# Optimization experiments

Hardware: AMD Instinct MI355X
Metric: run time of the kernel (lower is better)

The kernel has to match this reference:

```python
import jax, jax.numpy as jnp
import numpy as np

RESO = 64
VSIZE = 0.3
VOXEL = VSIZE / RESO
HALF = VOXEL / 2.0


def _voxel_xyz():
    line = (np.arange(RESO, dtype=np.float32) * VOXEL + HALF)
    x, y, z = np.meshgrid(line, line, line, indexing='ij')
    return jnp.asarray(np.stack([x, y, z]))  # [3,R,R,R]


def _grid_sample_2d(feats, gx, gy):
    # feats: [NV,C,H,W]; gx,gy: [NV,N] normalized coords (torch align_corners-style)
    NV, C, H, W = feats.shape
    ix = (gx + 1.0) * 0.5 * (W - 1)
    iy = (gy + 1.0) * 0.5 * (H - 1)
    ix0 = jnp.floor(ix); iy0 = jnp.floor(iy)
    ix1 = ix0 + 1.0;     iy1 = iy0 + 1.0
    # bilinear weights from unclamped corners
    w_nw = (ix1 - ix) * (iy1 - iy)
    w_ne = (ix - ix0) * (iy1 - iy)
    w_sw = (ix1 - ix) * (iy - iy0)
    w_se = (ix - ix0) * (iy - iy0)
    mask = ((ix >= 0) & (ix <= W - 1) & (iy >= 0) & (iy <= H - 1)).astype(feats.dtype)
    cx0 = jnp.clip(ix0, 0, W - 1).astype(jnp.int32)
    cx1 = jnp.clip(ix1, 0, W - 1).astype(jnp.int32)
    cy0 = jnp.clip(iy0, 0, H - 1).astype(jnp.int32)
    cy1 = jnp.clip(iy1, 0, H - 1).astype(jnp.int32)
    feats_flat = feats.reshape(NV, C, H * W)  # [NV,C,HW]
    gather = jax.vmap(lambda f, i: f[:, i])   # per-view [C,HW],[N] -> [C,N]
    v_nw = gather(feats_flat, cy0 * W + cx0)
    v_ne = gather(feats_flat, cy0 * W + cx1)
    v_sw = gather(feats_flat, cy1 * W + cx0)
    v_se = gather(feats_flat, cy1 * W + cx1)
    out = (v_nw * w_nw[:, None] + v_ne * w_ne[:, None]
           + v_sw * w_sw[:, None] + v_se * w_se[:, None])  # [NV,C,N]
    return out, mask


def setup_inputs() -> dict:
    key = jax.random.key(0)
    k_feat, k1, k2, k3 = jax.random.split(key, 4)
    NV, C, H, W = 8, 32, 128, 128
    feats = jax.random.normal(k_feat, (NV, C, H, W), dtype=jnp.float32)
    # realistic pinhole intrinsics for a 512x512 image
    K = np.array([[400.0, 0.0, 256.0], [0.0, 400.0, 256.0], [0.0, 0.0, 1.0]], np.float32)
    Ks = jnp.asarray(np.tile(K, (NV, 1, 1)))
    # identity-rotation w2c poses, camera ~0.5m from volume along +z
    poses = []
    for i in range(NV):
        t = np.array([0.02 * (i - 3.5), 0.01 * (i % 2), 0.5 + 0.02 * i], np.float32)
        poses.append(np.concatenate([np.eye(3, dtype=np.float32), t[:, None]], axis=1))
    ref_poses = jnp.asarray(np.stack(poses))
    bbox = jnp.asarray(np.array([[-0.15, -0.15, 0.0], [0.15, 0.15, 0.3]], np.float32))
    W1 = jax.random.normal(k1, (32, 32), dtype=jnp.float32) * 0.1
    W2 = jax.random.normal(k2, (32, 16), dtype=jnp.float32) * 0.1
    W3 = jax.random.normal(k3, (16, 8), dtype=jnp.float32) * 0.1
    return {"feats": feats, "ref_poses": ref_poses, "Ks": Ks, "bbox": bbox,
            "img_h": 512, "img_w": 512,
            "W1": W1, "b1": jnp.zeros((32,), jnp.float32),
            "W2": W2, "b2": jnp.zeros((16,), jnp.float32),
            "W3": W3, "b3": jnp.zeros((8,), jnp.float32)}


def reference(feats, ref_poses, Ks, bbox, img_h, img_w, W1, b1, W2, b2, W3, b3):
    NV, C, H, W = feats.shape
    dt = feats.dtype
    # homogeneous pad of poses and intrinsics
    pose_h = jnp.tile(jnp.eye(4, dtype=dt), (NV, 1, 1)).at[:, :3, :4].set(ref_poses)
    K_pad = jnp.tile(jnp.eye(4, dtype=dt), (NV, 1, 1)).at[:, :3, :3].set(Ks)
    w2pixel = K_pad @ pose_h  # [NV,4,4]
    # voxel centers in world frame
    xyz = _voxel_xyz() + bbox[0][:, None, None, None]  # [3,R,R,R]
    pts = xyz.reshape(3, -1)                            # [3,N], N=R^3
    homo = jnp.concatenate([pts, jnp.ones_like(pts[0:1])], axis=0)  # [4,N]
    pix = jnp.einsum('vij,jn->vin', w2pixel, homo)[:, :3]           # [NV,3,N]
    z = pix[:, 2]                                                    # [NV,N]
    mask_valid_depth = (z > 0).astype(dt)
    uv = pix[:, :2] / z[:, None, :]                                  # [NV,2,N]
    normalizer = jnp.array([img_w, img_h], dtype=dt)
    grid = uv.transpose(0, 2, 1) / normalizer - 1.0                  # [NV,N,2]
    feat, mask = _grid_sample_2d(feats, grid[..., 0], grid[..., 1])  # [NV,C,N],[NV,N]
    mask = mask * mask_valid_depth
    # [NV,C,(X Y Z)] -> [NV,X,Y,Z,C]
    feat = feat.transpose(0, 2, 1).reshape(NV, RESO, RESO, RESO, C)
    mask = mask.reshape(NV, RESO, RESO, RESO)
    # NOTE: original normalizes over dim=1 (NumX), replicated faithfully
    weight = mask / (jnp.sum(mask, axis=1, keepdims=True) + 1e-8)
    weight = weight[..., None]  # [NV,R,R,R,1]
    h1 = jax.nn.relu(feat @ W1 + b1)
    h2 = jax.nn.relu(h1 @ W2 + b2)
    comp = h2 @ W3 + b3  # [NV,R,R,R,8]
    mean = jnp.sum(comp * weight, axis=0, keepdims=True)
    var = jnp.sum(weight * (comp - mean) ** 2, axis=0, keepdims=True)
    mv = jnp.concatenate([mean, var], axis=-1)       # [1,R,R,R,16]
    return jnp.transpose(mv, (0, 4, 3, 2, 1))        # [1,16,Z,Y,X]
```

## Files before the change

### kernel.cpp

```cpp
#include <hip/hip_runtime.h>
#include <math.h>

#define NVIEW 8
#define CIN   32
#define HF    128
#define WF    128
#define C1    32
#define C2    16
#define C3    8
#define RESO  64
#define PLANE (HF*WF)

typedef _Float16 half8_t  __attribute__((ext_vector_type(8)));
typedef _Float16 half2_t  __attribute__((ext_vector_type(2)));
typedef float    floatx4  __attribute__((ext_vector_type(4)));

static __device__ __forceinline__ float vox_coord(int idx, float b) {
    const float VOXEL = (float)(0.3 / 64.0);
    const float HALFV = (float)(0.3 / 128.0);
    return (float)idx * VOXEL + HALFV + b;
}

static __device__ __forceinline__ void proj_ixiy(const float* M, float x, float y, float z,
                                                 float& ix, float& iy, float& zc) {
    float u  = fmaf(M[0], x, fmaf(M[1], y, fmaf(M[2],  z, M[3])));
    float vv = fmaf(M[4], x, fmaf(M[5], y, fmaf(M[6],  z, M[7])));
    zc       = fmaf(M[8], x, fmaf(M[9], y, fmaf(M[10], z, M[11])));
    float invz = __builtin_amdgcn_rcpf(zc);
    ix = u * invz;
    iy = vv * invz;
}

static __device__ __forceinline__ void wave_lds_sync() {
    asm volatile("s_waitcnt lgkmcnt(0)" ::: "memory");
}

__global__ void __launch_bounds__(256) k_g(const float* __restrict__ feats,
                                           const float* __restrict__ W1,
                                           const float* __restrict__ b1,
                                           float4* __restrict__ G4,
                                           const float* __restrict__ Ks,
                                           const float* __restrict__ poses,
                                           const int* __restrict__ ihp,
                                           const int* __restrict__ iwp,
                                           const float* __restrict__ W2,
                                           const float* __restrict__ b2,
                                           const float* __restrict__ W3,
                                           const float* __restrict__ b3,
                                           float* __restrict__ mats,
                                           _Float16* __restrict__ w2f,
                                           _Float16* __restrict__ w3f,
                                           float* __restrict__ b2f,
                                           float* __restrict__ b3f) {
    if (blockIdx.x == 512) {
        int t = threadIdx.x;
        if (t < NVIEW * 12) {
            int v = t / 12, rc = t % 12, r = rc / 4, c = rc % 4;
            const float* K = Ks + v * 9;
            const float* P = poses + v * 12;
            float s = K[r*3+0]*P[0*4+c] + K[r*3+1]*P[1*4+c] + K[r*3+2]*P[2*4+c];
            float sc = (r == 0) ? 63.5f / (float)iwp[0]
                     : (r == 1) ? 63.5f / (float)ihp[0] : 1.0f;
            mats[v*12 + r*4 + c] = s * sc;
        }
        if (t < 64) {
            int n = t & 15, g = t >> 4;
#pragma unroll
            for (int jj = 0; jj < 8; jj++) {
                int kk = 8 * g + jj;
                w2f[t*8 + jj] = (_Float16)W2[kk * C2 + n];
                float w3v = (kk < C2 && n < C3) ? W3[kk * C3 + n] : 0.0f;
                w3f[t*8 + jj] = (_Float16)w3v;
            }
            b2f[t] = b2[n];
            b3f[t] = (n < C3) ? b3[n] : 0.0f;
        }
        return;
    }
    int t = blockIdx.x * 256 + threadIdx.x;
    int pix = t & (PLANE - 1);
    int v = t >> 14;
    const float* fp = feats + ((size_t)v * CIN) * PLANE + pix;
    float f[CIN];
#pragma unroll
    for (int c = 0; c < CIN; c++) f[c] = fp[(size_t)c * PLANE];
    float g[C1];
#pragma unroll
    for (int jj = 0; jj < C1; jj++) g[jj] = b1[jj];
#pragma unroll
    for (int c = 0; c < CIN; c++) {
        float fc = f[c];
#pragma unroll
        for (int jj = 0; jj < C1; jj++) g[jj] = fmaf(fc, W1[c*C1 + jj], g[jj]);
    }
#pragma unroll
    for (int q = 0; q < C1/4; q++)
        G4[((size_t)(v * 8 + q)) * PLANE + pix] =
            make_float4(g[4*q], g[4*q+1], g[4*q+2], g[4*q+3]);
}

__global__ void __launch_bounds__(256) k_main(
    const float4* __restrict__ G4,
    const float* __restrict__ mats, const float* __restrict__ bbox,
    const _Float16* __restrict__ w2f, const _Float16* __restrict__ w3f,
    const float* __restrict__ b2f, const float* __restrict__ b3f,
    float* __restrict__ out) {
    __shared__ __align__(16) _Float16 h2s[4][64 * 24];

    int tid  = threadIdx.x;
    int wv   = tid >> 6;
    int lane = tid & 63;
    int col  = blockIdx.x * 4 + wv;
    int j  = col & 63;
    int kz = col >> 6;
    _Float16* h2b = h2s[wv];

    int m = lane & 15, g = lane >> 4;
    float y = vox_coord(j, bbox[1]);
    float z = vox_coord(kz, bbox[2]);

    half8_t w2frag = *(const half8_t*)(w2f + lane * 8);
    half8_t w3frag = *(const half8_t*)(w3f + lane * 8);
    float b2c = b2f[lane];
    float b3c = b3f[lane];
    floatx4 cb2 = {b2c, b2c, b2c, b2c};
    floatx4 cb3 = {b3c, b3c, b3c, b3c};

    float M1[16], Msq[16], S16[16];
#pragma unroll
    for (int c = 0; c < 16; c++) { M1[c] = 0.0f; Msq[c] = 0.0f; S16[c] = 0.0f; }

#pragma unroll 1
    for (int v = 0; v < NVIEW; v++) {
        const float* M = mats + v * 12;
        const float4* Gv = G4 + (size_t)v * 8 * PLANE;

        floatx4 c2v[4];
        unsigned int ballo[4];
        int popc = 0;

#pragma unroll
        for (int T = 0; T < 4; T++) {
            int ipt = T * 16 + m;
            float x = vox_coord(ipt, bbox[0]);
            float ix, iy, zc;
            proj_ixiy(M, x, y, z, ix, iy, zc);

            float fx0 = floorf(ix), fy0 = floorf(iy);
            float fx1 = fx0 + 1.0f, fy1 = fy0 + 1.0f;
            bool inb = (ix >= 0.0f) && (ix <= (float)(WF-1)) &&
                       (iy >= 0.0f) && (iy <= (float)(HF-1)) && (zc > 0.0f);
            int cx0 = (int)fminf(fmaxf(fx0, 0.0f), (float)(WF-1));
            int cx1 = (int)fminf(fmaxf(fx1, 0.0f), (float)(WF-1));
            int cy0 = (int)fminf(fmaxf(fy0, 0.0f), (float)(HF-1));
            int cy1 = (int)fminf(fmaxf(fy1, 0.0f), (float)(HF-1));
            float wnw = (fx1 - ix) * (fy1 - iy);
            float wne = (ix - fx0) * (fy1 - iy);
            float wsw = (fx1 - ix) * (iy - fy0);
            float wse = (ix - fx0) * (iy - fy0);

            unsigned long long bal = __ballot(inb);
            ballo[T] = (unsigned int)bal;
            popc += __popcll(bal);

            int t00 = cy0 * WF + cx0, t01 = cy0 * WF + cx1;
            int t10 = cy1 * WF + cx0, t11 = cy1 * WF + cx1;
            const float4* P0 = Gv + (2*g)     * PLANE;
            const float4* P1 = Gv + (2*g + 1) * PLANE;
            float4 a0 = P0[t00], b0 = P0[t01], c0 = P0[t10], d0 = P0[t11];
            float4 a1 = P1[t00], b1v = P1[t01], c1 = P1[t10], d1 = P1[t11];

            float e0 = fmaxf(fmaf(wnw, a0.x, fmaf(wne, b0.x, fmaf(wsw, c0.x, wse * d0.x))), 0.0f);
            float e1 = fmaxf(fmaf(wnw, a0.y, fmaf(wne, b0.y, fmaf(wsw, c0.y, wse * d0.y))), 0.0f);
            float e2 = fmaxf(fmaf(wnw, a0.z, fmaf(wne, b0.z, fmaf(wsw, c0.z, wse * d0.z))), 0.0f);
            float e3 = fmaxf(fmaf(wnw, a0.w, fmaf(wne, b0.w, fmaf(wsw, c0.w, wse * d0.w))), 0.0f);
            float e4 = fmaxf(fmaf(wnw, a1.x, fmaf(wne, b1v.x, fmaf(wsw, c1.x, wse * d1.x))), 0.0f);
            float e5 = fmaxf(fmaf(wnw, a1.y, fmaf(wne, b1v.y, fmaf(wsw, c1.y, wse * d1.y))), 0.0f);
            float e6 = fmaxf(fmaf(wnw, a1.z, fmaf(wne, b1v.z, fmaf(wsw, c1.z, wse * d1.z))), 0.0f);
            float e7 = fmaxf(fmaf(wnw, a1.w, fmaf(wne, b1v.w, fmaf(wsw, c1.w, wse * d1.w))), 0.0f);

            union { half8_t h8; half2_t h2[4]; } u;
            u.h2[0] = __builtin_bit_cast(half2_t, __builtin_amdgcn_cvt_pkrtz(e0, e1));
            u.h2[1] = __builtin_bit_cast(half2_t, __builtin_amdgcn_cvt_pkrtz(e2, e3));
            u.h2[2] = __builtin_bit_cast(half2_t, __builtin_amdgcn_cvt_pkrtz(e4, e5));
            u.h2[3] = __builtin_bit_cast(half2_t, __builtin_amdgcn_cvt_pkrtz(e6, e7));

            c2v[T] = __builtin_amdgcn_mfma_f32_16x16x32_f16(u.h8, w2frag, cb2, 0, 0, 0);
        }

        wave_lds_sync();
#pragma unroll
        for (int T = 0; T < 4; T++) {
#pragma unroll
            for (int r = 0; r < 4; r++) {
                float vv = fmaxf(c2v[T][r], 0.0f);
                h2b[(T*16 + g*4 + r) * 24 + m] = (_Float16)vv;
            }
        }
        wave_lds_sync();

        float msr = __builtin_amdgcn_rcpf((float)(popc >> 2) + 1e-8f);
#pragma unroll
        for (int T = 0; T < 4; T++) {
            half8_t a3 = *(const half8_t*)(h2b + (T*16 + m) * 24 + (g & 1) * 8);
            floatx4 c3 = __builtin_amdgcn_mfma_f32_16x16x32_f16(a3, w3frag, cb3, 0, 0, 0);
#pragma unroll
            for (int r = 0; r < 4; r++) {
                float w = ((ballo[T] >> (g*4 + r)) & 1u) ? msr : 0.0f;
                float val = c3[r];
                float t1 = w * val;
                S16[T*4+r] += w;
                M1[T*4+r]  += t1;
                Msq[T*4+r]  = fmaf(t1, val, Msq[T*4+r]);
            }
        }
    }

    if (m < C3) {
        size_t base = (size_t)col * 64;
#pragma unroll
        for (int T = 0; T < 4; T++) {
            float4 mn, vr;
            mn.x = M1[T*4+0]; mn.y = M1[T*4+1]; mn.z = M1[T*4+2]; mn.w = M1[T*4+3];
            vr.x = fmaf(mn.x*mn.x, S16[T*4+0]-2.0f, Msq[T*4+0]);
            vr.y = fmaf(mn.y*mn.y, S16[T*4+1]-2.0f, Msq[T*4+1]);
            vr.z = fmaf(mn.z*mn.z, S16[T*4+2]-2.0f, Msq[T*4+2]);
            vr.w = fmaf(mn.w*mn.w, S16[T*4+3]-2.0f, Msq[T*4+3]);
            size_t ob = base + T*16 + g*4;
            *(float4*)(out + (size_t)m       * 262144 + ob) = mn;
            *(float4*)(out + (size_t)(m + 8) * 262144 + ob) = vr;
        }
    }
}

extern "C" void kernel_launch(void* const* d_in, const int* in_sizes, int n_in,
                              void* d_out, int out_size, void* d_ws, size_t ws_size,
                              hipStream_t stream) {
    const float* feats = (const float*)d_in[0];
    const float* poses = (const float*)d_in[1];
    const float* Ks    = (const float*)d_in[2];
    const float* bbox  = (const float*)d_in[3];
    const int*   img_h = (const int*)d_in[4];
    const int*   img_w = (const int*)d_in[5];
    const float* W1    = (const float*)d_in[6];
    const float* b1    = (const float*)d_in[7];
    const float* W2    = (const float*)d_in[8];
    const float* b2    = (const float*)d_in[9];
    const float* W3    = (const float*)d_in[10];
    const float* b3    = (const float*)d_in[11];
    float* out = (float*)d_out;
    float* ws  = (float*)d_ws;

    float*     mats = ws;
    _Float16*  w2f  = (_Float16*)(ws + 128);
    _Float16*  w3f  = (_Float16*)(ws + 384);
    float*     b2f  = ws + 640;
    float*     b3f  = ws + 704;
    float4*    G4   = (float4*)(ws + 768);

    hipLaunchKernelGGL(k_g, dim3(513), dim3(256), 0, stream,
                       feats, W1, b1, G4, Ks, poses, img_h, img_w,
                       W2, b2, W3, b3, mats, w2f, w3f, b2f, b3f);
    hipLaunchKernelGGL(k_main, dim3(1024), dim3(256), 0, stream,
                       G4, mats, bbox, w2f, w3f, b2f, b3f, out);
}
```

Baseline: 142.3 us.

## Split each voxel column across two waves and double the grid

Each wave now handles 32 x-voxels of a column instead of 64, so two waves share one column and the grid doubles to 2048 blocks. The per-column mask count is recomputed per wave with a cheap single projection and ballot over all 64 lanes, and the mask bit is read from that 64-bit ballot. This halves per-thread register arrays and per-wave serial work to raise occupancy and latency hiding. In exchange, the projection and view-loop overhead is duplicated across the two waves.

```diff
diff --git a/kernel.cpp b/kernel.cpp
--- a/kernel.cpp
+++ b/kernel.cpp
@@ -105,12 +105,14 @@
     const _Float16* __restrict__ w2f, const _Float16* __restrict__ w3f,
     const float* __restrict__ b2f, const float* __restrict__ b3f,
     float* __restrict__ out) {
-    __shared__ __align__(16) _Float16 h2s[4][64 * 24];
+    __shared__ __align__(16) _Float16 h2s[4][32 * 24];
 
     int tid  = threadIdx.x;
     int wv   = tid >> 6;
     int lane = tid & 63;
-    int col  = blockIdx.x * 4 + wv;
+    int col  = blockIdx.x * 2 + (wv >> 1);
+    int half = wv & 1;
+    int w32  = half * 32;
     int j  = col & 63;
     int kz = col >> 6;
     _Float16* h2b = h2s[wv];
@@ -118,6 +120,10 @@
     int m = lane & 15, g = lane >> 4;
     float y = vox_coord(j, bbox[1]);
     float z = vox_coord(kz, bbox[2]);
+    float xmask = vox_coord(lane, bbox[0]);
+    float xb[2];
+    xb[0] = vox_coord(w32 + m,      bbox[0]);
+    xb[1] = vox_coord(w32 + 16 + m, bbox[0]);
 
     half8_t w2frag = *(const half8_t*)(w2f + lane * 8);
     half8_t w3frag = *(const half8_t*)(w3f + lane * 8);
@@ -126,30 +132,30 @@
     floatx4 cb2 = {b2c, b2c, b2c, b2c};
     floatx4 cb3 = {b3c, b3c, b3c, b3c};
 
-    float M1[16], Msq[16], S16[16];
-#pragma unroll
-    for (int c = 0; c < 16; c++) { M1[c] = 0.0f; Msq[c] = 0.0f; S16[c] = 0.0f; }
+    float M1[8], Msq[8], S16[8];
+#pragma unroll
+    for (int c = 0; c < 8; c++) { M1[c] = 0.0f; Msq[c] = 0.0f; S16[c] = 0.0f; }
 
 #pragma unroll 1
     for (int v = 0; v < NVIEW; v++) {
         const float* M = mats + v * 12;
         const float4* Gv = G4 + (size_t)v * 8 * PLANE;
 
-        floatx4 c2v[4];
-        unsigned int ballo[4];
-        int popc = 0;
-
-#pragma unroll
-        for (int T = 0; T < 4; T++) {
-            int ipt = T * 16 + m;
-            float x = vox_coord(ipt, bbox[0]);
+        float ixm, iym, zcm;
+        proj_ixiy(M, xmask, y, z, ixm, iym, zcm);
+        bool inbm = (ixm >= 0.0f) && (ixm <= (float)(WF-1)) &&
+                    (iym >= 0.0f) && (iym <= (float)(HF-1)) && (zcm > 0.0f);
+        unsigned long long bal = __ballot(inbm);
+        float msr = __builtin_amdgcn_rcpf((float)__popcll(bal) + 1e-8f);
+
+        floatx4 c2v[2];
+#pragma unroll
+        for (int T = 0; T < 2; T++) {
             float ix, iy, zc;
-            proj_ixiy(M, x, y, z, ix, iy, zc);
+            proj_ixiy(M, xb[T], y, z, ix, iy, zc);
 
             float fx0 = floorf(ix), fy0 = floorf(iy);
             float fx1 = fx0 + 1.0f, fy1 = fy0 + 1.0f;
-            bool inb = (ix >= 0.0f) && (ix <= (float)(WF-1)) &&
-                       (iy >= 0.0f) && (iy <= (float)(HF-1)) && (zc > 0.0f);
             int cx0 = (int)fminf(fmaxf(fx0, 0.0f), (float)(WF-1));
             int cx1 = (int)fminf(fmaxf(fx1, 0.0f), (float)(WF-1));
             int cy0 = (int)fminf(fmaxf(fy0, 0.0f), (float)(HF-1));
@@ -159,10 +165,6 @@
             float wsw = (fx1 - ix) * (iy - fy0);
             float wse = (ix - fx0) * (iy - fy0);
 
-            unsigned long long bal = __ballot(inb);
-            ballo[T] = (unsigned int)bal;
-            popc += __popcll(bal);
-
             int t00 = cy0 * WF + cx0, t01 = cy0 * WF + cx1;
             int t10 = cy1 * WF + cx0, t11 = cy1 * WF + cx1;
             const float4* P0 = Gv + (2*g)     * PLANE;
@@ -190,7 +192,7 @@
 
         wave_lds_sync();
 #pragma unroll
-        for (int T = 0; T < 4; T++) {
+        for (int T = 0; T < 2; T++) {
 #pragma unroll
             for (int r = 0; r < 4; r++) {
                 float vv = fmaxf(c2v[T][r], 0.0f);
@@ -199,14 +201,14 @@
         }
         wave_lds_sync();
 
-        float msr = __builtin_amdgcn_rcpf((float)(popc >> 2) + 1e-8f);
-#pragma unroll
-        for (int T = 0; T < 4; T++) {
+#pragma unroll
+        for (int T = 0; T < 2; T++) {
             half8_t a3 = *(const half8_t*)(h2b + (T*16 + m) * 24 + (g & 1) * 8);
             floatx4 c3 = __builtin_amdgcn_mfma_f32_16x16x32_f16(a3, w3frag, cb3, 0, 0, 0);
 #pragma unroll
             for (int r = 0; r < 4; r++) {
-                float w = ((ballo[T] >> (g*4 + r)) & 1u) ? msr : 0.0f;
+                int gp = w32 + T*16 + g*4 + r;
+                float w = ((bal >> gp) & 1ull) ? msr : 0.0f;
                 float val = c3[r];
                 float t1 = w * val;
                 S16[T*4+r] += w;
@@ -217,9 +219,9 @@
     }
 
     if (m < C3) {
-        size_t base = (size_t)col * 64;
-#pragma unroll
-        for (int T = 0; T < 4; T++) {
+        size_t base = (size_t)col * 64 + w32;
+#pragma unroll
+        for (int T = 0; T < 2; T++) {
             float4 mn, vr;
             mn.x = M1[T*4+0]; mn.y = M1[T*4+1]; mn.z = M1[T*4+2]; mn.w = M1[T*4+3];
             vr.x = fmaf(mn.x*mn.x, S16[T*4+0]-2.0f, Msq[T*4+0]);
@@ -261,6 +263,6 @@
     hipLaunchKernelGGL(k_g, dim3(513), dim3(256), 0, stream,
                        feats, W1, b1, G4, Ks, poses, img_h, img_w,
                        W2, b2, W3, b3, mats, w2f, w3f, b2f, b3f);
-    hipLaunchKernelGGL(k_main, dim3(1024), dim3(256), 0, stream,
+    hipLaunchKernelGGL(k_main, dim3(2048), dim3(256), 0, stream,
                        G4, mats, bbox, w2f, w3f, b2f, b3f, out);
 }
```

Result: slower. 152.7 us (+7.3%).
